# Optimization experiments

Measured on AMD Instinct MI355X. Metric: run time of the kernel, lower is better.

## Reference

```python
import jax, jax.numpy as jnp
import numpy as np

B, T, D, H, E, M = 4, 2048, 2048, 8, 512, 8  # batch, seq, hidden, moe_heads, moe_experts, moe_dim//2
F = E * M  # flatten_shape = 4096
HALF = D // 2


def act(z):
    # 'relu2' activation: relu(x)**2
    r = jax.nn.relu(z)
    return r * r


def setup_inputs() -> dict:
    key = jax.random.key(0)
    ks = jax.random.split(key, 13)
    s = 0.02
    return {
        "x": jax.random.normal(ks[0], (B, T, D), jnp.float32),
        "g1": jax.random.uniform(ks[1], (B, T, H, E), jnp.float32),
        "g2": jax.random.uniform(ks[2], (B, T, H, E), jnp.float32),
        "u1_w": jax.random.normal(ks[3], (F, D), jnp.float32) * s,
        "u1_b": jnp.zeros((F,), jnp.float32),
        "u2_w": jax.random.normal(ks[4], (F, D), jnp.float32) * s,
        "u2_b": jnp.zeros((F,), jnp.float32),
        "v11_w": jax.random.normal(ks[5], (HALF, F), jnp.float32) * s,
        "v12_w": jax.random.normal(ks[6], (HALF, F), jnp.float32) * s,
        "v21_w": jax.random.normal(ks[7], (HALF, F), jnp.float32) * s,
        "v22_w": jax.random.normal(ks[8], (HALF, F), jnp.float32) * s,
        "b1": jax.random.normal(ks[9], (E, HALF), jnp.float32) * s,
        "b2": jax.random.normal(ks[10], (E, HALF), jnp.float32) * s,
    }


def reference(x, g1, g2, u1_w, u1_b, u2_w, u2_b, v11_w, v12_w, v21_w, v22_w, b1, b2):
    # x1, x2: [B,T,E,M]
    x1 = act(x @ u1_w.T + u1_b).reshape(B, T, E, M)
    x2 = act(x @ u2_w.T + u2_b).reshape(B, T, E, M)

    g1s = g1.sum(axis=2)  # [B,T,E] (einsum '...hi->...i')
    g2s = g2.sum(axis=2)

    # x11 = v11(einsum('btim,bthi->btim', x1, g1).flatten(-2))
    x11 = (x1 * g1s[..., None]).reshape(B, T, F) @ v11_w.T
    # x12 = v12(einsum('btjm,bthj,bthi->btim', x2, g2, g1).flatten(-2))
    t2 = jnp.einsum('btjm,bthj->bthm', x2, g2)
    x12 = jnp.einsum('bthm,bthi->btim', t2, g1).reshape(B, T, F) @ v12_w.T
    # x13 = einsum('bthi,id->btd', g1, b1)
    x13 = g1s @ b1

    # x21 = v21(einsum('btim,bthi,bthj->btjm', x1, g1, g2).flatten(-2))
    t1 = jnp.einsum('btim,bthi->bthm', x1, g1)
    x21 = jnp.einsum('bthm,bthj->btjm', t1, g2).reshape(B, T, F) @ v21_w.T
    # x22 = v22(einsum('btjm,bthj->btjm', x2, g2).flatten(-2))
    x22 = (x2 * g2s[..., None]).reshape(B, T, F) @ v22_w.T
    # x23 = einsum('bthj,jd->btd', g2, b2)
    x23 = g2s @ b2

    return jnp.concatenate((x11 + x12 + x13, x21 + x22 + x23), axis=-1)
```

## Files before the change

### kernel.cpp

```cpp
#include <hip/hip_runtime.h>
#include <hip/hip_bf16.h>

#define TOK   8192
#define DD    2048
#define FF    4096
#define EE    512
#define HALF  1024
#define KCAT  8704

typedef __bf16 bf16x8 __attribute__((ext_vector_type(8)));
typedef __bf16 bf16x4 __attribute__((ext_vector_type(4)));
typedef float  f32x4  __attribute__((ext_vector_type(4)));
using bf16 = __hip_bfloat16;

#define AS1(p) ((const __attribute__((address_space(1))) void*)(p))
#define AS3(p) ((__attribute__((address_space(3))) void*)(p))


__global__ void cvt_bf16(const float* __restrict__ in, bf16* __restrict__ out, int n4) {
    int i = blockIdx.x * blockDim.x + threadIdx.x;
    int stride = gridDim.x * blockDim.x;
    for (; i < n4; i += stride) {
        float4 v = ((const float4*)in)[i];
        bf16x4 o;
        o[0] = (__bf16)v.x; o[1] = (__bf16)v.y; o[2] = (__bf16)v.z; o[3] = (__bf16)v.w;
        ((bf16x4*)out)[i] = o;
    }
}

__global__ void pack_w(const float* __restrict__ vA, const float* __restrict__ vB,
                       const float* __restrict__ bmat, bf16* __restrict__ W) {
    int n = blockIdx.x;
    const float* ra = vA + (size_t)n * FF;
    const float* rb = vB + (size_t)n * FF;
    bf16* w = W + (size_t)n * KCAT;
    for (int k = threadIdx.x; k < FF; k += 256) {
        w[k]      = __float2bfloat16(ra[k]);
        w[FF + k] = __float2bfloat16(rb[k]);
    }
    for (int e = threadIdx.x; e < EE; e += 256)
        w[2 * FF + e] = __float2bfloat16(bmat[(size_t)e * HALF + n]);
}

template<int MODE>
__global__ __launch_bounds__(512, 2)
void gemmR(const bf16* __restrict__ A0, const bf16* __restrict__ B0,
           const float* __restrict__ bias0, void* __restrict__ C0,
           const bf16* __restrict__ A1, const bf16* __restrict__ B1,
           const float* __restrict__ bias1, void* __restrict__ C1,
           int nbm, int nbn, int K, int ldc)
{
    __shared__ __align__(16) char smem[131072];
    const int tid  = threadIdx.x;
    const int lane = tid & 63;
    const int wid  = tid >> 6;
    const int wm = wid >> 2, wn = wid & 3;
    const int r16 = lane & 15, kb = lane >> 4;

    int bid = blockIdx.x;
    {
        int nwg = gridDim.x;
        int q = nwg >> 3, r = nwg & 7;
        int xcd = bid & 7, idx = bid >> 3;
        bid = (xcd < r ? xcd * (q + 1) : r * (q + 1) + (xcd - r) * q) + idx;
    }
    const int npg = nbm * nbn;
    const int g   = bid / npg;
    const int lb  = bid - g * npg;
    const int bm = lb / nbn, bn = lb - bm * nbn;

    const bf16*  A    = g ? A1 : A0;
    const bf16*  Bw   = g ? B1 : B0;
    const float* bias = g ? bias1 : bias0;
    char* Cout = (char*)(g ? C1 : C0);

    const long row0 = (long)bm * 256;
    const int  col0 = bn * 256;
    const int  nt   = K >> 6;

    const char* gA[2]; const char* gB[2];
    #pragma unroll
    for (int l = 0; l < 2; ++l) {
        const uint32_t S = (uint32_t)(l * 512 + tid) * 16;
        const int r  = (int)(S >> 6);
        const int cb = (int)((S & 63) ^ ((uint32_t)((r >> 1) & 3) << 4));
        gA[l] = (const char*)A  + (row0 + r) * (long)K * 2 + cb;
        gB[l] = (const char*)Bw + (long)(col0 + r) * K * 2 + cb;
    }
    const uint32_t ldst = (uint32_t)(tid & ~63) * 16;

    const uint32_t swz  = ((uint32_t)(r16 >> 1) & 3u) << 4;
    const uint32_t aoff = (uint32_t)((wm * 128 + r16) * 64 + kb * 16) ^ swz;
    const uint32_t boff = (uint32_t)((wn * 64  + r16) * 64 + kb * 16) ^ swz;

    f32x4 acc[8][4];
    #pragma unroll
    for (int i = 0; i < 8; ++i)
        #pragma unroll
        for (int j = 0; j < 4; ++j)
            acc[i][j] = (f32x4){0.f, 0.f, 0.f, 0.f};

#define STAGEK(BUFOFF, KOFF)                                                             \
    __builtin_amdgcn_global_load_lds(AS1(gA[0] + (KOFF)), AS3(smem + (BUFOFF) +     0 + ldst), 16, 0, 0); \
    __builtin_amdgcn_global_load_lds(AS1(gA[1] + (KOFF)), AS3(smem + (BUFOFF) +  8192 + ldst), 16, 0, 0); \
    __builtin_amdgcn_global_load_lds(AS1(gB[0] + (KOFF)), AS3(smem + (BUFOFF) + 32768 + ldst), 16, 0, 0); \
    __builtin_amdgcn_global_load_lds(AS1(gB[1] + (KOFF)), AS3(smem + (BUFOFF) + 40960 + ldst), 16, 0, 0);

#define READS(AF, BV, PB, PLOFF)                                                         \
    _Pragma("unroll")                                                                    \
    for (int fi = 0; fi < 8; ++fi) AF[fi] = *(const bf16x8*)((PB) + (PLOFF) + aoff + fi * 1024); \
    _Pragma("unroll")                                                                    \
    for (int fj = 0; fj < 4; ++fj) BV[fj] = *(const bf16x8*)((PB) + (PLOFF) + 32768 + boff + fj * 1024);

#define MFMA32(AF, BV)                                                                   \
    __builtin_amdgcn_s_setprio(1);                                                       \
    _Pragma("unroll")                                                                    \
    for (int fi = 0; fi < 8; ++fi) {                                                     \
        _Pragma("unroll")                                                                \
        for (int fj = 0; fj < 4; ++fj)                                                   \
            acc[fi][fj] = __builtin_amdgcn_mfma_f32_16x16x32_bf16(AF[fi], BV[fj], acc[fi][fj], 0, 0, 0); \
    }                                                                                    \
    __builtin_amdgcn_s_setprio(0);

    STAGEK(0, 0)
    STAGEK(16384, 64)
    asm volatile("s_waitcnt vmcnt(4)\n\ts_barrier" ::: "memory");

    bf16x8 af0[8], bv0[4], af1[8], bv1[4];
    READS(af0, bv0, smem, 0)

    for (int t = 0; t < nt; ++t) {
        const uint32_t bo  = ((uint32_t)(t & 1)) << 16;
        const uint32_t bo1 = bo ^ 65536u;
        const char* pb = smem + bo;
        const char* pt = smem + bo1;
        const bool  st = (t + 1 < nt);
        const long  k1 = (long)(t + 1) * 128;

        if (st) { STAGEK(bo1, k1) }
        if (st) asm volatile("s_waitcnt vmcnt(4)" ::: "memory");
        else    asm volatile("s_waitcnt vmcnt(0)" ::: "memory");
        asm volatile("s_barrier" ::: "memory");
        READS(af1, bv1, pb, 16384)
        MFMA32(af0, bv0)

        if (st) {
            STAGEK(bo1 + 16384, k1 + 64)
            asm volatile("s_waitcnt vmcnt(4)" ::: "memory");
        }
        asm volatile("s_barrier" ::: "memory");
        if (st) { READS(af0, bv0, pt, 0) }
        MFMA32(af1, bv1)
    }
#undef MFMA32
#undef READS
#undef STAGEK

    const int rb = (lane >> 4) * 4;
    #pragma unroll
    for (int i = 0; i < 8; ++i) {
        #pragma unroll
        for (int j = 0; j < 4; ++j) {
            const int cc = col0 + wn * 64 + j * 16 + r16;
            float badd = 0.f;
            if (MODE == 1) badd = bias[cc];
            #pragma unroll
            for (int e = 0; e < 4; ++e) {
                long row = row0 + wm * 128 + i * 16 + rb + e;
                float v = acc[i][j][e];
                if (MODE == 1) {
                    v += badd;
                    v = fmaxf(v, 0.f);
                    v = v * v;
                    ((bf16*)Cout)[row * ldc + cc] = __float2bfloat16(v);
                } else {
                    ((float*)Cout)[row * ldc + cc] = v;
                }
            }
        }
    }
}

#define GPAD 524
__global__ __launch_bounds__(256)
void glue(const float* __restrict__ g1, const float* __restrict__ g2,
          bf16* __restrict__ Yl, bf16* __restrict__ Yr)
{
    __shared__ __align__(16) float g1t[8 * GPAD];
    __shared__ __align__(16) float g2t[8 * GPAD];
    __shared__ float g1s[EE], g2s[EE];
    __shared__ float t1s[64], t2s[64];
    __shared__ float t1p[4][64], t2p[4][64];
    __shared__ __align__(16) bf16 x1t[FF], x2t[FF];

    const int t   = blockIdx.x;
    const int tid = threadIdx.x;
    const float* g1p = g1 + (size_t)t * FF;
    const float* g2p = g2 + (size_t)t * FF;
    bf16* ylp = Yl + (size_t)t * KCAT;
    bf16* yrp = Yr + (size_t)t * KCAT;

    #pragma unroll
    for (int c = 0; c < 4; ++c) {
        int idx4 = (c * 256 + tid) * 4;
        float4 v1 = *(const float4*)(g1p + idx4);
        float4 v2 = *(const float4*)(g2p + idx4);
        int h = idx4 >> 9, e = idx4 & 511;
        *(float4*)&g1t[h * GPAD + e] = v1;
        *(float4*)&g2t[h * GPAD + e] = v2;
    }
    #pragma unroll
    for (int c = 0; c < 2; ++c) {
        int idx8 = (c * 256 + tid) * 8;
        *(bf16x8*)&x1t[idx8] = *(const bf16x8*)(ylp + idx8);
        *(bf16x8*)&x2t[idx8] = *(const bf16x8*)(yrp + FF + idx8);
    }
    __syncthreads();

    #pragma unroll
    for (int c = 0; c < 2; ++c) {
        int e = c * 256 + tid;
        float s1 = 0.f, s2 = 0.f;
        #pragma unroll
        for (int h = 0; h < 8; ++h) { s1 += g1t[h * GPAD + e]; s2 += g2t[h * GPAD + e]; }
        g1s[e] = s1; g2s[e] = s2;
    }

    {
        int o = tid & 63;
        int h = o & 7, m = o >> 3;
        int p = tid >> 6;
        float s1 = 0.f, s2 = 0.f;
        #pragma unroll 8
        for (int ii = 0; ii < 128; ++ii) {
            int e = p * 128 + ii;
            float xv1 = __bfloat162float(x1t[e * 8 + m]);
            float xv2 = __bfloat162float(x2t[e * 8 + m]);
            s1 += xv1 * g1t[h * GPAD + e];
            s2 += xv2 * g2t[h * GPAD + e];
        }
        t1p[p][o] = s1; t2p[p][o] = s2;
    }
    __syncthreads();
    if (tid < 64)       t1s[tid] = t1p[0][tid] + t1p[1][tid] + t1p[2][tid] + t1p[3][tid];
    else if (tid < 128) { int o = tid - 64; t2s[o] = t2p[0][o] + t2p[1][o] + t2p[2][o] + t2p[3][o]; }
    __syncthreads();

    #pragma unroll
    for (int c = 0; c < 2; ++c) {
        int f0 = (c * 256 + tid) * 8;
        int e  = f0 >> 3;
        float s1 = g1s[e], s2 = g2s[e];
        bf16x8 xa = *(const bf16x8*)&x1t[f0];
        bf16x8 xb = *(const bf16x8*)&x2t[f0];
        bf16x8 o1, o2;
        #pragma unroll
        for (int u = 0; u < 8; ++u) {
            o1[u] = (__bf16)((float)xa[u] * s1);
            o2[u] = (__bf16)((float)xb[u] * s2);
        }
        *(bf16x8*)(ylp + f0)      = o1;
        *(bf16x8*)(yrp + FF + f0) = o2;
    }
    #pragma unroll
    for (int c = 0; c < 2; ++c) {
        int f0 = (c * 256 + tid) * 8;
        int i  = f0 >> 3;
        bf16x8 o12v, o21v;
        #pragma unroll
        for (int m = 0; m < 8; ++m) {
            float s12 = 0.f, s21 = 0.f;
            #pragma unroll
            for (int h = 0; h < 8; ++h) {
                s12 += t2s[(m << 3) | h] * g1t[h * GPAD + i];
                s21 += t1s[(m << 3) | h] * g2t[h * GPAD + i];
            }
            o12v[m] = (__bf16)s12;
            o21v[m] = (__bf16)s21;
        }
        *(bf16x8*)(ylp + FF + f0) = o12v;
        *(bf16x8*)(yrp + f0)      = o21v;
    }
    {
        int e0 = tid * 2;
        ylp[2 * FF + e0]     = __float2bfloat16(g1s[e0]);
        ylp[2 * FF + e0 + 1] = __float2bfloat16(g1s[e0 + 1]);
        yrp[2 * FF + e0]     = __float2bfloat16(g2s[e0]);
        yrp[2 * FF + e0 + 1] = __float2bfloat16(g2s[e0 + 1]);
    }
}


extern "C" void kernel_launch(void* const* d_in, const int* in_sizes, int n_in,
                              void* d_out, int out_size, void* d_ws, size_t ws_size,
                              hipStream_t stream) {
    const float* x    = (const float*)d_in[0];
    const float* g1   = (const float*)d_in[1];
    const float* g2   = (const float*)d_in[2];
    const float* u1_w = (const float*)d_in[3];
    const float* u1_b = (const float*)d_in[4];
    const float* u2_w = (const float*)d_in[5];
    const float* u2_b = (const float*)d_in[6];
    const float* v11  = (const float*)d_in[7];
    const float* v12  = (const float*)d_in[8];
    const float* v21  = (const float*)d_in[9];
    const float* v22  = (const float*)d_in[10];
    const float* b1   = (const float*)d_in[11];
    const float* b2   = (const float*)d_in[12];
    float* out = (float*)d_out;

    size_t off = 0;
    char* base = (char*)d_ws;
    auto take = [&](size_t bytes) { void* p = base + off; off += (bytes + 255) & ~(size_t)255; return p; };
    bf16* Xb  = (bf16*)take((size_t)TOK * DD * 2);
    bf16* U1b = (bf16*)take((size_t)FF * DD * 2);
    bf16* U2b = (bf16*)take((size_t)FF * DD * 2);
    bf16* Wl  = (bf16*)take((size_t)HALF * KCAT * 2);
    bf16* Wr  = (bf16*)take((size_t)HALF * KCAT * 2);
    bf16* Yl  = (bf16*)take((size_t)TOK * KCAT * 2);
    bf16* Yr  = (bf16*)take((size_t)TOK * KCAT * 2);

    cvt_bf16<<<4096, 256, 0, stream>>>(x,    Xb,  TOK * DD / 4);
    cvt_bf16<<<2048, 256, 0, stream>>>(u1_w, U1b, FF * DD / 4);
    cvt_bf16<<<2048, 256, 0, stream>>>(u2_w, U2b, FF * DD / 4);
    pack_w<<<HALF, 256, 0, stream>>>(v11, v12, b1, Wl);
    pack_w<<<HALF, 256, 0, stream>>>(v21, v22, b2, Wr);

    gemmR<1><<<2 * (TOK / 256) * (FF / 256), 512, 0, stream>>>(
        Xb, U1b, u1_b, Yl,
        Xb, U2b, u2_b, Yr + FF,
        TOK / 256, FF / 256, DD, KCAT);

    glue<<<TOK, 256, 0, stream>>>(g1, g2, Yl, Yr);

    gemmR<0><<<2 * (TOK / 256) * (HALF / 256), 512, 0, stream>>>(
        Yl, Wl, nullptr, out,
        Yr, Wr, nullptr, out + HALF,
        TOK / 256, HALF / 256, KCAT, DD);
}
```

Measured before the change: 726.7 us.

## Rewrite GEMM with 32x32x16 MFMA and four-phase interleaved LDS pipeline

Replaces the 16x16x32 bf16 MFMA tiling with 32x32x16 MFMAs on 4x2 f32x16 accumulators per wave. The main loop is reorganised into four barrier-separated quadrants that interleave partial global-to-LDS staging with fragment reads and MFMA bursts, with a 128-wide K tile per buffer. The goal is fewer LDS reads per FLOP and better overlap of loads with compute. Launch bounds drop to one block per CU, and the many barriers could add sync overhead.

```diff
diff --git a/kernel.cpp b/kernel.cpp
--- a/kernel.cpp
+++ b/kernel.cpp
@@ -11,6 +11,7 @@
 typedef __bf16 bf16x8 __attribute__((ext_vector_type(8)));
 typedef __bf16 bf16x4 __attribute__((ext_vector_type(4)));
 typedef float  f32x4  __attribute__((ext_vector_type(4)));
+typedef float  f32x16 __attribute__((ext_vector_type(16)));
 using bf16 = __hip_bfloat16;
 
 #define AS1(p) ((const __attribute__((address_space(1))) void*)(p))
@@ -43,8 +44,8 @@
 }
 
 template<int MODE>
-__global__ __launch_bounds__(512, 2)
-void gemmR(const bf16* __restrict__ A0, const bf16* __restrict__ B0,
+__global__ __launch_bounds__(512, 1)
+void gemmS(const bf16* __restrict__ A0, const bf16* __restrict__ B0,
            const float* __restrict__ bias0, void* __restrict__ C0,
            const bf16* __restrict__ A1, const bf16* __restrict__ B1,
            const float* __restrict__ bias1, void* __restrict__ C1,
@@ -55,7 +56,7 @@
     const int lane = tid & 63;
     const int wid  = tid >> 6;
     const int wm = wid >> 2, wn = wid & 3;
-    const int r16 = lane & 15, kb = lane >> 4;
+    const int l31 = lane & 31, kh = lane >> 5;
 
     int bid = blockIdx.x;
     {
@@ -89,85 +90,137 @@
     }
     const uint32_t ldst = (uint32_t)(tid & ~63) * 16;
 
-    const uint32_t swz  = ((uint32_t)(r16 >> 1) & 3u) << 4;
-    const uint32_t aoff = (uint32_t)((wm * 128 + r16) * 64 + kb * 16) ^ swz;
-    const uint32_t boff = (uint32_t)((wn * 64  + r16) * 64 + kb * 16) ^ swz;
-
-    f32x4 acc[8][4];
-    #pragma unroll
-    for (int i = 0; i < 8; ++i)
-        #pragma unroll
-        for (int j = 0; j < 4; ++j)
-            acc[i][j] = (f32x4){0.f, 0.f, 0.f, 0.f};
-
-#define STAGEK(BUFOFF, KOFF)                                                             \
-    __builtin_amdgcn_global_load_lds(AS1(gA[0] + (KOFF)), AS3(smem + (BUFOFF) +     0 + ldst), 16, 0, 0); \
-    __builtin_amdgcn_global_load_lds(AS1(gA[1] + (KOFF)), AS3(smem + (BUFOFF) +  8192 + ldst), 16, 0, 0); \
-    __builtin_amdgcn_global_load_lds(AS1(gB[0] + (KOFF)), AS3(smem + (BUFOFF) + 32768 + ldst), 16, 0, 0); \
-    __builtin_amdgcn_global_load_lds(AS1(gB[1] + (KOFF)), AS3(smem + (BUFOFF) + 40960 + ldst), 16, 0, 0);
-
-#define READS(AF, BV, PB, PLOFF)                                                         \
-    _Pragma("unroll")                                                                    \
-    for (int fi = 0; fi < 8; ++fi) AF[fi] = *(const bf16x8*)((PB) + (PLOFF) + aoff + fi * 1024); \
-    _Pragma("unroll")                                                                    \
-    for (int fj = 0; fj < 4; ++fj) BV[fj] = *(const bf16x8*)((PB) + (PLOFF) + 32768 + boff + fj * 1024);
-
-#define MFMA32(AF, BV)                                                                   \
-    __builtin_amdgcn_s_setprio(1);                                                       \
-    _Pragma("unroll")                                                                    \
-    for (int fi = 0; fi < 8; ++fi) {                                                     \
-        _Pragma("unroll")                                                                \
-        for (int fj = 0; fj < 4; ++fj)                                                   \
-            acc[fi][fj] = __builtin_amdgcn_mfma_f32_16x16x32_bf16(AF[fi], BV[fj], acc[fi][fj], 0, 0, 0); \
-    }                                                                                    \
+    const uint32_t swz = ((uint32_t)(lane >> 1) & 3u) << 4;
+    const uint32_t cs0 = ((uint32_t)(kh << 4)) ^ swz;
+    const uint32_t cs1 = ((uint32_t)(32 | (kh << 4))) ^ swz;
+    const uint32_t aBase = (uint32_t)(wm * 128 + l31) * 64;
+    const uint32_t bBase = 32768u + (uint32_t)(wn * 64 + l31) * 64;
+
+    f32x16 acc[4][2];
+    #pragma unroll
+    for (int i = 0; i < 4; ++i)
+        #pragma unroll
+        for (int j = 0; j < 2; ++j)
+            acc[i][j] = (f32x16)(0.f);
+
+#define ST_AH0(BUF, KOFF)                                                                 \
+    __builtin_amdgcn_global_load_lds(AS1(gA[0] + (KOFF)),      AS3(smem + (BUF) +     0 + ldst), 16, 0, 0); \
+    __builtin_amdgcn_global_load_lds(AS1(gA[0] + (KOFF) + 64), AS3(smem + (BUF) + 16384 + ldst), 16, 0, 0);
+#define ST_AH1(BUF, KOFF)                                                                 \
+    __builtin_amdgcn_global_load_lds(AS1(gA[1] + (KOFF)),      AS3(smem + (BUF) +  8192 + ldst), 16, 0, 0); \
+    __builtin_amdgcn_global_load_lds(AS1(gA[1] + (KOFF) + 64), AS3(smem + (BUF) + 24576 + ldst), 16, 0, 0);
+#define ST_BH0(BUF, KOFF)                                                                 \
+    __builtin_amdgcn_global_load_lds(AS1(gB[0] + (KOFF)),      AS3(smem + (BUF) + 32768 + ldst), 16, 0, 0); \
+    __builtin_amdgcn_global_load_lds(AS1(gB[0] + (KOFF) + 64), AS3(smem + (BUF) + 49152 + ldst), 16, 0, 0);
+#define ST_BH1(BUF, KOFF)                                                                 \
+    __builtin_amdgcn_global_load_lds(AS1(gB[1] + (KOFF)),      AS3(smem + (BUF) + 40960 + ldst), 16, 0, 0); \
+    __builtin_amdgcn_global_load_lds(AS1(gB[1] + (KOFF) + 64), AS3(smem + (BUF) + 57344 + ldst), 16, 0, 0);
+
+#define RD_A(DST, PB, FIB)                                                                \
+    _Pragma("unroll")                                                                     \
+    for (int ks = 0; ks < 4; ++ks) {                                                      \
+        _Pragma("unroll")                                                                 \
+        for (int f = 0; f < 2; ++f)                                                       \
+            DST[f * 4 + ks] = *(const bf16x8*)((PB) + ((ks >> 1) << 14) + aBase           \
+                                               + ((FIB) + f) * 2048 + ((ks & 1) ? cs1 : cs0)); \
+    }
+#define RD_B(DST, PB, FJ)                                                                 \
+    _Pragma("unroll")                                                                     \
+    for (int ks = 0; ks < 4; ++ks)                                                        \
+        DST[ks] = *(const bf16x8*)((PB) + ((ks >> 1) << 14) + bBase + (FJ) * 2048         \
+                                   + ((ks & 1) ? cs1 : cs0));
+
+#define QUAD(AF, BV, FI0, FJ)                                                             \
+    asm volatile("s_waitcnt lgkmcnt(0)" ::: "memory");                                    \
+    __builtin_amdgcn_sched_barrier(0);                                                    \
+    __builtin_amdgcn_s_setprio(1);                                                        \
+    _Pragma("unroll")                                                                     \
+    for (int ks = 0; ks < 4; ++ks) {                                                      \
+        _Pragma("unroll")                                                                 \
+        for (int f = 0; f < 2; ++f)                                                       \
+            acc[(FI0) + f][FJ] = __builtin_amdgcn_mfma_f32_32x32x16_bf16(                 \
+                AF[f * 4 + ks], BV[ks], acc[(FI0) + f][FJ], 0, 0, 0);                     \
+    }                                                                                     \
     __builtin_amdgcn_s_setprio(0);
 
-    STAGEK(0, 0)
-    STAGEK(16384, 64)
-    asm volatile("s_waitcnt vmcnt(4)\n\ts_barrier" ::: "memory");
-
-    bf16x8 af0[8], bv0[4], af1[8], bv1[4];
-    READS(af0, bv0, smem, 0)
+#define BAR() asm volatile("s_barrier" ::: "memory");
+
+    bf16x8 afA[8], afB[8], bv0[4], bv1[4];
+
+    ST_AH0(0u, 0) ST_AH1(0u, 0) ST_BH0(0u, 0) ST_BH1(0u, 0)
+    if (nt > 1) {
+        ST_AH0(65536u, 128)
+        asm volatile("s_waitcnt vmcnt(2)" ::: "memory");
+    } else {
+        asm volatile("s_waitcnt vmcnt(0)" ::: "memory");
+    }
+    BAR()
+    RD_A(afA, smem, 0)
 
     for (int t = 0; t < nt; ++t) {
         const uint32_t bo  = ((uint32_t)(t & 1)) << 16;
         const uint32_t bo1 = bo ^ 65536u;
         const char* pb = smem + bo;
         const char* pt = smem + bo1;
-        const bool  st = (t + 1 < nt);
+        const bool  s1 = (t + 1 < nt);
+        const bool  s2 = (t + 2 < nt);
         const long  k1 = (long)(t + 1) * 128;
-
-        if (st) { STAGEK(bo1, k1) }
-        if (st) asm volatile("s_waitcnt vmcnt(4)" ::: "memory");
-        else    asm volatile("s_waitcnt vmcnt(0)" ::: "memory");
-        asm volatile("s_barrier" ::: "memory");
-        READS(af1, bv1, pb, 16384)
-        MFMA32(af0, bv0)
-
-        if (st) {
-            STAGEK(bo1 + 16384, k1 + 64)
+        const long  k2 = (long)(t + 2) * 128;
+
+        RD_B(bv0, pb, 0)
+        if (s1) { ST_AH1(bo1, k1) }
+        BAR()
+        QUAD(afA, bv0, 0, 0)
+        BAR()
+
+        RD_B(bv1, pb, 1)
+        if (s1) { ST_BH0(bo1, k1) }
+        BAR()
+        QUAD(afA, bv1, 0, 1)
+        BAR()
+
+        RD_A(afB, pb, 2)
+        if (s1) {
+            ST_BH1(bo1, k1)
             asm volatile("s_waitcnt vmcnt(4)" ::: "memory");
         }
-        asm volatile("s_barrier" ::: "memory");
-        if (st) { READS(af0, bv0, pt, 0) }
-        MFMA32(af1, bv1)
-    }
-#undef MFMA32
-#undef READS
-#undef STAGEK
-
-    const int rb = (lane >> 4) * 4;
-    #pragma unroll
-    for (int i = 0; i < 8; ++i) {
-        #pragma unroll
-        for (int j = 0; j < 4; ++j) {
-            const int cc = col0 + wn * 64 + j * 16 + r16;
+        BAR()
+        QUAD(afB, bv0, 2, 0)
+        BAR()
+
+        if (s1) { RD_A(afA, pt, 0) }
+        if (s2) {
+            ST_AH0(bo, k2)
+            asm volatile("s_waitcnt vmcnt(2)" ::: "memory");
+        } else if (s1) {
+            asm volatile("s_waitcnt vmcnt(0)" ::: "memory");
+        }
+        BAR()
+        QUAD(afB, bv1, 2, 1)
+        BAR()
+    }
+#undef QUAD
+#undef RD_A
+#undef RD_B
+#undef ST_AH0
+#undef ST_AH1
+#undef ST_BH0
+#undef ST_BH1
+#undef BAR
+
+    const int rowb = wm * 128 + kh * 4;
+    const int colb = col0 + wn * 64 + l31;
+    #pragma unroll
+    for (int i = 0; i < 4; ++i) {
+        #pragma unroll
+        for (int j = 0; j < 2; ++j) {
+            const int cc = colb + j * 32;
             float badd = 0.f;
             if (MODE == 1) badd = bias[cc];
             #pragma unroll
-            for (int e = 0; e < 4; ++e) {
-                long row = row0 + wm * 128 + i * 16 + rb + e;
-                float v = acc[i][j][e];
+            for (int rg = 0; rg < 16; ++rg) {
+                long row = row0 + rowb + i * 32 + (rg & 3) + 8 * (rg >> 2);
+                float v = acc[i][j][rg];
                 if (MODE == 1) {
                     v += badd;
                     v = fmaxf(v, 0.f);
@@ -326,14 +379,14 @@
     pack_w<<<HALF, 256, 0, stream>>>(v11, v12, b1, Wl);
     pack_w<<<HALF, 256, 0, stream>>>(v21, v22, b2, Wr);
 
-    gemmR<1><<<2 * (TOK / 256) * (FF / 256), 512, 0, stream>>>(
+    gemmS<1><<<2 * (TOK / 256) * (FF / 256), 512, 0, stream>>>(
         Xb, U1b, u1_b, Yl,
         Xb, U2b, u2_b, Yr + FF,
         TOK / 256, FF / 256, DD, KCAT);
 
     glue<<<TOK, 256, 0, stream>>>(g1, g2, Yl, Yr);
 
-    gemmR<0><<<2 * (TOK / 256) * (HALF / 256), 512, 0, stream>>>(
+    gemmS<0><<<2 * (TOK / 256) * (HALF / 256), 512, 0, stream>>>(
         Yl, Wl, nullptr, out,
         Yr, Wr, nullptr, out + HALF,
         TOK / 256, HALF / 256, KCAT, DD);
```

Measured after the change: 744.1 us. +2.4%, slower.

## Use 4-wave GEMM blocks with 128x128 warp tiles and simpler staging

Applied to the files above, without the earlier changes.

The GEMM kernel moves from 8 waves of 512 threads to 4 waves of 256 threads. Each wave now computes a 128x128 output tile (8x8 MFMA accumulators) instead of 128x64, so each LDS fragment is reused more and LDS read traffic per FLOP drops. The pipeline goes from two half-K stages with fragment double-buffering to one full 128-K stage per iteration, with a single barrier and all fragments read before the MFMAs. This raises register pressure: 256 accumulator floats plus 32 fragment registers per lane, which needs AGPRs and allows one block per CU. Less LDS-read/MFMA overlap within a wave is also a risk.

```diff
diff --git a/kernel.cpp b/kernel.cpp
--- a/kernel.cpp
+++ b/kernel.cpp
@@ -43,8 +43,8 @@
 }
 
 template<int MODE>
-__global__ __launch_bounds__(512, 2)
-void gemmR(const bf16* __restrict__ A0, const bf16* __restrict__ B0,
+__global__ __launch_bounds__(256, 1)
+void gemmW(const bf16* __restrict__ A0, const bf16* __restrict__ B0,
            const float* __restrict__ bias0, void* __restrict__ C0,
            const bf16* __restrict__ A1, const bf16* __restrict__ B1,
            const float* __restrict__ bias1, void* __restrict__ C1,
@@ -54,7 +54,7 @@
     const int tid  = threadIdx.x;
     const int lane = tid & 63;
     const int wid  = tid >> 6;
-    const int wm = wid >> 2, wn = wid & 3;
+    const int wm = wid >> 1, wn = wid & 1;
     const int r16 = lane & 15, kb = lane >> 4;
 
     int bid = blockIdx.x;
@@ -78,90 +78,88 @@
     const int  col0 = bn * 256;
     const int  nt   = K >> 6;
 
-    const char* gA[2]; const char* gB[2];
-    #pragma unroll
-    for (int l = 0; l < 2; ++l) {
-        const uint32_t S = (uint32_t)(l * 512 + tid) * 16;
+    const char* gA; const char* gB;
+    {
+        const uint32_t S = (uint32_t)tid * 16;
         const int r  = (int)(S >> 6);
         const int cb = (int)((S & 63) ^ ((uint32_t)((r >> 1) & 3) << 4));
-        gA[l] = (const char*)A  + (row0 + r) * (long)K * 2 + cb;
-        gB[l] = (const char*)Bw + (long)(col0 + r) * K * 2 + cb;
-    }
+        gA = (const char*)A  + (row0 + r) * (long)K * 2 + cb;
+        gB = (const char*)Bw + (long)(col0 + r) * K * 2 + cb;
+    }
+    const long lstep = 64L * K * 2;
     const uint32_t ldst = (uint32_t)(tid & ~63) * 16;
+
+#define STAGE(BUF, KOFF)                                                                  \
+    _Pragma("unroll")                                                                     \
+    for (int l = 0; l < 4; ++l) {                                                         \
+        __builtin_amdgcn_global_load_lds(AS1(gA + l * lstep + (KOFF)),                    \
+            AS3(smem + (BUF) +     0 + l * 4096 + ldst), 16, 0, 0);                       \
+        __builtin_amdgcn_global_load_lds(AS1(gA + l * lstep + (KOFF) + 64),               \
+            AS3(smem + (BUF) + 16384 + l * 4096 + ldst), 16, 0, 0);                       \
+        __builtin_amdgcn_global_load_lds(AS1(gB + l * lstep + (KOFF)),                    \
+            AS3(smem + (BUF) + 32768 + l * 4096 + ldst), 16, 0, 0);                       \
+        __builtin_amdgcn_global_load_lds(AS1(gB + l * lstep + (KOFF) + 64),               \
+            AS3(smem + (BUF) + 49152 + l * 4096 + ldst), 16, 0, 0);                       \
+    }
 
     const uint32_t swz  = ((uint32_t)(r16 >> 1) & 3u) << 4;
     const uint32_t aoff = (uint32_t)((wm * 128 + r16) * 64 + kb * 16) ^ swz;
-    const uint32_t boff = (uint32_t)((wn * 64  + r16) * 64 + kb * 16) ^ swz;
-
-    f32x4 acc[8][4];
+    const uint32_t boff = (uint32_t)((wn * 128 + r16) * 64 + kb * 16) ^ swz;
+
+    f32x4 acc[8][8];
     #pragma unroll
     for (int i = 0; i < 8; ++i)
         #pragma unroll
-        for (int j = 0; j < 4; ++j)
+        for (int j = 0; j < 8; ++j)
             acc[i][j] = (f32x4){0.f, 0.f, 0.f, 0.f};
 
-#define STAGEK(BUFOFF, KOFF)                                                             \
-    __builtin_amdgcn_global_load_lds(AS1(gA[0] + (KOFF)), AS3(smem + (BUFOFF) +     0 + ldst), 16, 0, 0); \
-    __builtin_amdgcn_global_load_lds(AS1(gA[1] + (KOFF)), AS3(smem + (BUFOFF) +  8192 + ldst), 16, 0, 0); \
-    __builtin_amdgcn_global_load_lds(AS1(gB[0] + (KOFF)), AS3(smem + (BUFOFF) + 32768 + ldst), 16, 0, 0); \
-    __builtin_amdgcn_global_load_lds(AS1(gB[1] + (KOFF)), AS3(smem + (BUFOFF) + 40960 + ldst), 16, 0, 0);
-
-#define READS(AF, BV, PB, PLOFF)                                                         \
-    _Pragma("unroll")                                                                    \
-    for (int fi = 0; fi < 8; ++fi) AF[fi] = *(const bf16x8*)((PB) + (PLOFF) + aoff + fi * 1024); \
-    _Pragma("unroll")                                                                    \
-    for (int fj = 0; fj < 4; ++fj) BV[fj] = *(const bf16x8*)((PB) + (PLOFF) + 32768 + boff + fj * 1024);
-
-#define MFMA32(AF, BV)                                                                   \
-    __builtin_amdgcn_s_setprio(1);                                                       \
-    _Pragma("unroll")                                                                    \
-    for (int fi = 0; fi < 8; ++fi) {                                                     \
-        _Pragma("unroll")                                                                \
-        for (int fj = 0; fj < 4; ++fj)                                                   \
-            acc[fi][fj] = __builtin_amdgcn_mfma_f32_16x16x32_bf16(AF[fi], BV[fj], acc[fi][fj], 0, 0, 0); \
-    }                                                                                    \
-    __builtin_amdgcn_s_setprio(0);
-
-    STAGEK(0, 0)
-    STAGEK(16384, 64)
-    asm volatile("s_waitcnt vmcnt(4)\n\ts_barrier" ::: "memory");
-
-    bf16x8 af0[8], bv0[4], af1[8], bv1[4];
-    READS(af0, bv0, smem, 0)
+    STAGE(0u, 0)
 
     for (int t = 0; t < nt; ++t) {
         const uint32_t bo  = ((uint32_t)(t & 1)) << 16;
         const uint32_t bo1 = bo ^ 65536u;
         const char* pb = smem + bo;
-        const char* pt = smem + bo1;
         const bool  st = (t + 1 < nt);
         const long  k1 = (long)(t + 1) * 128;
 
-        if (st) { STAGEK(bo1, k1) }
-        if (st) asm volatile("s_waitcnt vmcnt(4)" ::: "memory");
-        else    asm volatile("s_waitcnt vmcnt(0)" ::: "memory");
+        if (st) {
+            STAGE(bo1, k1)
+            asm volatile("s_waitcnt vmcnt(16)" ::: "memory");
+        } else {
+            asm volatile("s_waitcnt vmcnt(0)" ::: "memory");
+        }
         asm volatile("s_barrier" ::: "memory");
-        READS(af1, bv1, pb, 16384)
-        MFMA32(af0, bv0)
-
-        if (st) {
-            STAGEK(bo1 + 16384, k1 + 64)
-            asm volatile("s_waitcnt vmcnt(4)" ::: "memory");
-        }
-        asm volatile("s_barrier" ::: "memory");
-        if (st) { READS(af0, bv0, pt, 0) }
-        MFMA32(af1, bv1)
-    }
-#undef MFMA32
-#undef READS
-#undef STAGEK
+
+        bf16x8 a0[8], b0[8], a1[8], b1[8];
+        #pragma unroll
+        for (int f = 0; f < 8; ++f) {
+            a0[f] = *(const bf16x8*)(pb +     0 + aoff + f * 1024);
+            b0[f] = *(const bf16x8*)(pb + 32768 + boff + f * 1024);
+            a1[f] = *(const bf16x8*)(pb + 16384 + aoff + f * 1024);
+            b1[f] = *(const bf16x8*)(pb + 49152 + boff + f * 1024);
+        }
+
+        __builtin_amdgcn_s_setprio(1);
+        #pragma unroll
+        for (int fi = 0; fi < 8; ++fi)
+            #pragma unroll
+            for (int fj = 0; fj < 8; ++fj)
+                acc[fi][fj] = __builtin_amdgcn_mfma_f32_16x16x32_bf16(a0[fi], b0[fj], acc[fi][fj], 0, 0, 0);
+        #pragma unroll
+        for (int fi = 0; fi < 8; ++fi)
+            #pragma unroll
+            for (int fj = 0; fj < 8; ++fj)
+                acc[fi][fj] = __builtin_amdgcn_mfma_f32_16x16x32_bf16(a1[fi], b1[fj], acc[fi][fj], 0, 0, 0);
+        __builtin_amdgcn_s_setprio(0);
+    }
+#undef STAGE
 
     const int rb = (lane >> 4) * 4;
     #pragma unroll
     for (int i = 0; i < 8; ++i) {
         #pragma unroll
-        for (int j = 0; j < 4; ++j) {
-            const int cc = col0 + wn * 64 + j * 16 + r16;
+        for (int j = 0; j < 8; ++j) {
+            const int cc = col0 + wn * 128 + j * 16 + r16;
             float badd = 0.f;
             if (MODE == 1) badd = bias[cc];
             #pragma unroll
@@ -326,14 +324,14 @@
     pack_w<<<HALF, 256, 0, stream>>>(v11, v12, b1, Wl);
     pack_w<<<HALF, 256, 0, stream>>>(v21, v22, b2, Wr);
 
-    gemmR<1><<<2 * (TOK / 256) * (FF / 256), 512, 0, stream>>>(
+    gemmW<1><<<2 * (TOK / 256) * (FF / 256), 256, 0, stream>>>(
         Xb, U1b, u1_b, Yl,
         Xb, U2b, u2_b, Yr + FF,
         TOK / 256, FF / 256, DD, KCAT);
 
     glue<<<TOK, 256, 0, stream>>>(g1, g2, Yl, Yr);
 
-    gemmR<0><<<2 * (TOK / 256) * (HALF / 256), 512, 0, stream>>>(
+    gemmW<0><<<2 * (TOK / 256) * (HALF / 256), 256, 0, stream>>>(
         Yl, Wl, nullptr, out,
         Yr, Wr, nullptr, out + HALF,
         TOK / 256, HALF / 256, KCAT, DD);
```

Measured after the change: 790.5 us. 8.8% more time.
